# Kernel tuning notes

Hardware: AMD Instinct MI355X
Metric: run time of the kernel (lower is better)

## Reference

```python
import jax, jax.numpy as jnp
import numpy as np

WS = (7, 7)   # window size
SS = (3, 3)   # shift size
NH = 8        # num heads
DIM = 256
B_, H_, W_ = 16, 112, 112


def _rel_index(wh, ww):
    ch, cw = np.meshgrid(np.arange(wh), np.arange(ww), indexing='ij')
    cf = np.stack([ch, cw]).reshape(2, -1)
    rc = (cf[:, :, None] - cf[:, None, :]).transpose(1, 2, 0)
    rc[:, :, 0] += wh - 1
    rc[:, :, 1] += ww - 1
    rc[:, :, 0] *= 2 * ww - 1
    return rc.sum(-1).reshape(-1)


def _shift_mask(pH, pW, wh, ww, sh, sw):
    m = np.zeros((pH, pW))
    cnt = 0
    for h0, h1 in ((0, pH - wh), (pH - wh, pH - sh), (pH - sh, pH)):
        for w0, w1 in ((0, pW - ww), (pW - ww, pW - sw), (pW - sw, pW)):
            m[h0:h1, w0:w1] = cnt
            cnt += 1
    m = m.reshape(pH // wh, wh, pW // ww, ww).transpose(0, 2, 1, 3).reshape(-1, wh * ww)
    d = m[:, None, :] - m[:, :, None]  # (nW, N, N), [w,i,j] = m[w,j]-m[w,i]
    return np.where(d != 0, -100.0, 0.0).astype(np.float32)


def _partition(x, wh, ww):
    B, H, W, C = x.shape
    x = x.reshape(B, H // wh, wh, W // ww, ww, C).transpose(0, 1, 3, 2, 4, 5)
    return x.reshape(B * (H // wh) * (W // ww), wh * ww, C)


def _unpartition(x, B, H, W, wh, ww):
    C = x.shape[-1]
    x = x.reshape(B, H // wh, W // ww, wh, ww, C).transpose(0, 1, 3, 2, 4, 5)
    return x.reshape(B, H, W, C)


def setup_inputs() -> dict:
    key = jax.random.key(0)
    ks = jax.random.split(key, 12)
    D = DIM
    inp = {
        'Q': jax.random.normal(ks[0], (B_, H_, W_, D), jnp.float32),
        'K': jax.random.normal(ks[1], (B_, H_, W_, D), jnp.float32),
        'V': jax.random.normal(ks[2], (B_, H_, W_, D), jnp.float32),
        'Qw': jax.random.normal(ks[3], (D, D), jnp.float32) * 0.02,
        'Qb': jax.random.normal(ks[4], (D,), jnp.float32) * 0.02,
        'Kw': jax.random.normal(ks[5], (D, D), jnp.float32) * 0.02,
        'Kb': jax.random.normal(ks[6], (D,), jnp.float32) * 0.02,
        'Vw': jax.random.normal(ks[7], (D, D), jnp.float32) * 0.02,
        'Vb': jax.random.normal(ks[8], (D,), jnp.float32) * 0.02,
        'Pw': jax.random.normal(ks[9], (D, D), jnp.float32) * 0.02,
        'Pb': jax.random.normal(ks[10], (D,), jnp.float32) * 0.02,
        'rpb_table': jax.random.normal(ks[11], ((2 * WS[0] - 1) * (2 * WS[1] - 1), NH), jnp.float32) * 0.02,
        'rp_index': jnp.asarray(_rel_index(WS[0], WS[1]), jnp.int32),
    }
    return inp


def reference(Q, K, V, Qw, Qb, Kw, Kb, Vw, Vb, Pw, Pb, rpb_table, rp_index):
    wh, ww = WS
    nh = NH
    B, H, W, C = Q.shape
    N = wh * ww
    hd = C // nh
    pad_b = (wh - H % wh) % wh
    pad_r = (ww - W % ww) % ww
    if pad_b or pad_r:
        pad = ((0, 0), (0, pad_b), (0, pad_r), (0, 0))
        Q, K, V = jnp.pad(Q, pad), jnp.pad(K, pad), jnp.pad(V, pad)
    pH, pW = H + pad_b, W + pad_r
    sh = 0 if wh >= pH else SS[0]
    sw = 0 if ww >= pW else SS[1]
    shifted = (sh + sw) > 0
    if shifted:
        Q = jnp.roll(Q, (-sh, -sw), (1, 2))
        K = jnp.roll(K, (-sh, -sw), (1, 2))
        V = jnp.roll(V, (-sh, -sw), (1, 2))
    xq = _partition(Q, wh, ww)  # (B*nW, N, C)
    xk = _partition(K, wh, ww)
    xv = _partition(V, wh, ww)
    q = (xq @ Qw.T + Qb).reshape(-1, N, nh, hd).transpose(0, 2, 1, 3) * (hd ** -0.5)
    k = (xk @ Kw.T + Kb).reshape(-1, N, nh, hd).transpose(0, 2, 1, 3)
    v = (xv @ Vw.T + Vb).reshape(-1, N, nh, hd).transpose(0, 2, 1, 3)
    bias = rpb_table[rp_index].reshape(N, N, nh).transpose(2, 0, 1)  # (nh, N, N)
    attn = jnp.einsum('bhnd,bhmd->bhnm', q, k) + bias[None]
    if shifted:
        mask = jnp.asarray(_shift_mask(pH, pW, wh, ww, sh, sw))  # (nW, N, N)
        nW = (pH // wh) * (pW // ww)
        attn = attn.reshape(B, nW, nh, N, N) + mask[None, :, None]
        attn = attn.reshape(-1, nh, N, N)
    attn = jax.nn.softmax(attn, axis=-1)
    x = jnp.einsum('bhnm,bhmd->bhnd', attn, v).transpose(0, 2, 1, 3).reshape(-1, N, C)
    x = x @ Pw.T + Pb
    x = _unpartition(x, B, pH, pW, wh, ww)
    if shifted:
        x = jnp.roll(x, (sh, sw), (1, 2))
    return x[:, :H, :W, :]
```

## Files before the change

### kernel.cpp

```cpp
#include <hip/hip_runtime.h>


typedef short  bf16x4_t __attribute__((ext_vector_type(4)));
typedef short  bf16x8_t __attribute__((ext_vector_type(8)));
typedef float  f32x4_t  __attribute__((ext_vector_type(4)));
typedef int    i32x4_t  __attribute__((ext_vector_type(4)));

#define HH    112
#define WWDIM 112
#define NTOK  49
#define NWIN  4096
#define SHIFT 3

__device__ __forceinline__ unsigned short f2bf(float f) {
  unsigned u = __builtin_bit_cast(unsigned, f);
  u += 0x7FFFu + ((u >> 16) & 1u);
  return (unsigned short)(u >> 16);
}

__device__ __forceinline__ bf16x8_t ld8(const unsigned short* p) {
  return __builtin_bit_cast(bf16x8_t, *reinterpret_cast<const i32x4_t*>(p));
}

__device__ __forceinline__ bf16x4_t pack4(float a, float b, float c, float d) {
  union { unsigned short u[4]; bf16x4_t v; } t;
  t.u[0] = f2bf(a); t.u[1] = f2bf(b); t.u[2] = f2bf(c); t.u[3] = f2bf(d);
  return t.v;
}

__device__ __forceinline__ int swzi(int row, int col, int rowElems) {
  int by = col << 1;
  int sb = (((by >> 4) ^ (row & 7)) << 4) | (by & 15);
  return row * rowElems + (sb >> 1);
}

__global__ void prep_kernel(const float* __restrict__ Qw, const float* __restrict__ Kw,
                            const float* __restrict__ Vw, const float* __restrict__ Pw,
                            const float* __restrict__ rpb, const int* __restrict__ rpi,
                            unsigned short* __restrict__ wbf, float* __restrict__ biasT) {
  int idx = blockIdx.x * 256 + threadIdx.x;
  if (idx < 4 * 65536) {
    int which = idx >> 16, e = idx & 65535;
    const float* s = (which == 0) ? Qw : (which == 1) ? Kw : (which == 2) ? Vw : Pw;
    wbf[idx] = f2bf(s[e]);
  }
  if (idx < 8 * NTOK * NTOK) {
    int h = idx / (NTOK * NTOK), ij = idx % (NTOK * NTOK);
    int i = ij / NTOK, j = ij - (ij / NTOK) * NTOK;
    biasT[h * (NTOK * NTOK) + j * NTOK + i] = rpb[rpi[ij] * 8 + h];
  }
}

#define GLOAD(SRC)                                                            \
  do {                                                                        \
    _Pragma("unroll") for (int it = 0; it < 8; ++it) {                        \
      g[it] = ((wid + (it << 3)) < NTOK)                                      \
                  ? *reinterpret_cast<const float4*>((SRC) + goff[it])        \
                  : make_float4(0.f, 0.f, 0.f, 0.f);                          \
    }                                                                         \
  } while (0)

#define XWRITE()                                                              \
  do {                                                                        \
    _Pragma("unroll") for (int it = 0; it < 8; ++it) {                        \
      unsigned v0 = (unsigned)f2bf(g[it].x) | ((unsigned)f2bf(g[it].y) << 16);\
      unsigned v1 = (unsigned)f2bf(g[it].z) | ((unsigned)f2bf(g[it].w) << 16);\
      *reinterpret_cast<uint2*>(                                              \
          &Xs[swzi(wid + (it << 3), lane << 2, 256)]) = make_uint2(v0, v1);   \
    }                                                                         \
  } while (0)

#define WHOIST(PH)                                                            \
  do {                                                                        \
    const unsigned short* W_ = wbf + ((PH) << 16);                            \
    _Pragma("unroll") for (int ks = 0; ks < 8; ++ks)                          \
        _Pragma("unroll") for (int t = 0; t < 2; ++t)                         \
            bw[ks][t] =                                                       \
        ld8(&W_[(((wid << 5) + (t << 4) + lo) << 8) + (ks << 5) + kof]);      \
  } while (0)

__global__ __launch_bounds__(512, 2) void fused_kernel(
    const float* __restrict__ Qin, const float* __restrict__ Kin, const float* __restrict__ Vin,
    const float* __restrict__ Qbv, const float* __restrict__ Kbv, const float* __restrict__ Vbv,
    const float* __restrict__ Pbv,
    const unsigned short* __restrict__ wbf, const float* __restrict__ biasT,
    float* __restrict__ out) {
  __shared__ unsigned short Xs[64 * 256];

  const int blk = blockIdx.x, tid = threadIdx.x;
  const int lane = tid & 63, wid = tid >> 6;
  const int b = blk >> 8, wi = (blk >> 4) & 15, wj = blk & 15;
  const int lo = lane & 15, hi = lane >> 4;
  const int g4 = hi << 2, kof = hi << 3;

  unsigned goff[8];
#pragma unroll
  for (int it = 0; it < 8; ++it) {
    int row = wid + (it << 3);
    unsigned off = 0;
    if (row < NTOK) {
      int i = row / 7, j = row - i * 7;
      int h_ = wi * 7 + i + SHIFT; if (h_ >= HH) h_ -= HH;
      int w_ = wj * 7 + j + SHIFT; if (w_ >= WWDIM) w_ -= WWDIM;
      off = ((unsigned)((b * HH + h_) * WWDIM + w_) << 8) + (lane << 2);
    }
    goff[it] = off;
  }

  float4 g[8];
  bf16x8_t bw[8][2];
  bf16x4_t qf[2][4], kf[2][4], vf[4][2];

  GLOAD(Qin);
  WHOIST(0);
  XWRITE();
  __syncthreads();

#pragma unroll
  for (int ph = 0; ph < 2; ++ph) {
    GLOAD(ph == 0 ? Kin : Vin);
    f32x4_t acc[2][4];
#pragma unroll
    for (int a = 0; a < 2; ++a)
#pragma unroll
      for (int c = 0; c < 4; ++c) acc[a][c] = (f32x4_t){0.f, 0.f, 0.f, 0.f};
#pragma unroll
    for (int ks = 0; ks < 8; ++ks) {
      const int kk = (ks << 5) + kof;
      bf16x8_t xb[4];
#pragma unroll
      for (int nj = 0; nj < 4; ++nj) xb[nj] = ld8(&Xs[swzi((nj << 4) + lo, kk, 256)]);
#pragma unroll
      for (int mi = 0; mi < 2; ++mi)
#pragma unroll
        for (int nj = 0; nj < 4; ++nj)
          acc[mi][nj] = __builtin_amdgcn_mfma_f32_16x16x32_bf16(bw[ks][mi], xb[nj], acc[mi][nj], 0, 0, 0);
    }
    const float* bias = (ph == 0) ? Qbv : Kbv;
    const float scale = (ph == 0) ? 0.17677669529663687f : 1.0f;
    bf16x4_t (*dst)[4] = (ph == 0) ? qf : kf;
#pragma unroll
    for (int mi = 0; mi < 2; ++mi) {
      const float4 bb = *reinterpret_cast<const float4*>(bias + (wid << 5) + (mi << 4) + g4);
#pragma unroll
      for (int nj = 0; nj < 4; ++nj)
        dst[mi][nj] = pack4((acc[mi][nj][0] + bb.x) * scale, (acc[mi][nj][1] + bb.y) * scale,
                            (acc[mi][nj][2] + bb.z) * scale, (acc[mi][nj][3] + bb.w) * scale);
    }
    __syncthreads();
    WHOIST(ph + 1);
    XWRITE();
    __syncthreads();
  }

  {
    f32x4_t acc[4][2];
#pragma unroll
    for (int a = 0; a < 4; ++a)
#pragma unroll
      for (int c = 0; c < 2; ++c) acc[a][c] = (f32x4_t){0.f, 0.f, 0.f, 0.f};
#pragma unroll
    for (int ks = 0; ks < 8; ++ks) {
      const int kk = (ks << 5) + kof;
      bf16x8_t xa[4];
#pragma unroll
      for (int mi = 0; mi < 4; ++mi) xa[mi] = ld8(&Xs[swzi((mi << 4) + lo, kk, 256)]);
#pragma unroll
      for (int mi = 0; mi < 4; ++mi)
#pragma unroll
        for (int t = 0; t < 2; ++t)
          acc[mi][t] = __builtin_amdgcn_mfma_f32_16x16x32_bf16(xa[mi], bw[ks][t], acc[mi][t], 0, 0, 0);
    }
    float bbv[2];
#pragma unroll
    for (int t = 0; t < 2; ++t) bbv[t] = Vbv[(wid << 5) + (t << 4) + lo];
#pragma unroll
    for (int mi = 0; mi < 4; ++mi)
#pragma unroll
      for (int t = 0; t < 2; ++t)
        vf[mi][t] = pack4(acc[mi][t][0] + bbv[t], acc[mi][t][1] + bbv[t],
                          acc[mi][t][2] + bbv[t], acc[mi][t][3] + bbv[t]);
  }
  WHOIST(3);

  const bool wi15 = (wi == 15), wj15 = (wj == 15);
  unsigned kbi = 0, kbj = 0, kval = 0;
#pragma unroll
  for (int njk = 0; njk < 4; ++njk)
#pragma unroll
    for (int rg = 0; rg < 4; ++rg) {
      int kt = (njk << 4) + g4 + rg;
      if (kt < NTOK) {
        int ti = kt / 7, tj = kt - (kt / 7) * 7;
        unsigned bit = 1u << (njk * 4 + rg);
        kval |= bit;
        if (ti >= 4) kbi |= bit;
        if (tj >= 4) kbj |= bit;
      }
    }

  f32x4_t st[4][4];
  __builtin_amdgcn_s_setprio(1);
#pragma unroll
  for (int njk = 0; njk < 4; ++njk)
#pragma unroll
    for (int njq = 0; njq < 4; ++njq) {
      st[njk][njq] = __builtin_amdgcn_mfma_f32_16x16x16bf16_1k(
          kf[0][njk], qf[0][njq], (f32x4_t){0.f, 0.f, 0.f, 0.f}, 0, 0, 0);
      st[njk][njq] = __builtin_amdgcn_mfma_f32_16x16x16bf16_1k(
          kf[1][njk], qf[1][njq], st[njk][njq], 0, 0, 0);
    }
  __builtin_amdgcn_s_setprio(0);

  const float* bh = biasT + wid * (NTOK * NTOK);
  bf16x4_t pf[4][4];
#pragma unroll
  for (int njq = 0; njq < 4; ++njq) {
    const int qt = (njq << 4) + lo;
    const bool qv = qt < NTOK;
    const int sqt = qv ? qt : 0;
    const int qti = sqt / 7, qtj = sqt - (sqt / 7) * 7;
    const bool qbi = qti >= 4, qbj = qtj >= 4;
    float vals[4][4];
    float m = -3e38f;
#pragma unroll
    for (int njk = 0; njk < 4; ++njk)
#pragma unroll
      for (int rg = 0; rg < 4; ++rg) {
        const int bit = njk * 4 + rg;
        const int kt = (njk << 4) + g4 + rg;
        const bool valid = qv && ((kval >> bit) & 1u);
        float v = st[njk][njq][rg] + bh[(valid ? kt : 0) * NTOK + sqt];
        if (wi15 && (qbi != (bool)((kbi >> bit) & 1u))) v -= 100.f;
        if (wj15 && (qbj != (bool)((kbj >> bit) & 1u))) v -= 100.f;
        v = valid ? v : -1e30f;
        vals[njk][rg] = v;
        m = fmaxf(m, v);
      }
    m = fmaxf(m, __shfl_xor(m, 16));
    m = fmaxf(m, __shfl_xor(m, 32));
    float sum = 0.f;
#pragma unroll
    for (int njk = 0; njk < 4; ++njk)
#pragma unroll
      for (int rg = 0; rg < 4; ++rg) {
        const float e = __expf(vals[njk][rg] - m);
        vals[njk][rg] = e;
        sum += e;
      }
    sum += __shfl_xor(sum, 16);
    sum += __shfl_xor(sum, 32);
    const float inv = 1.f / sum;
#pragma unroll
    for (int njk = 0; njk < 4; ++njk)
      pf[njk][njq] = pack4(vals[njk][0] * inv, vals[njk][1] * inv,
                           vals[njk][2] * inv, vals[njk][3] * inv);
  }

  f32x4_t o[2][4];
#pragma unroll
  for (int a = 0; a < 2; ++a)
#pragma unroll
    for (int c = 0; c < 4; ++c) o[a][c] = (f32x4_t){0.f, 0.f, 0.f, 0.f};
  __builtin_amdgcn_s_setprio(1);
#pragma unroll
  for (int mi = 0; mi < 4; ++mi)
#pragma unroll
    for (int t = 0; t < 2; ++t)
#pragma unroll
      for (int njq = 0; njq < 4; ++njq)
        o[t][njq] = __builtin_amdgcn_mfma_f32_16x16x16bf16_1k(vf[mi][t], pf[mi][njq], o[t][njq], 0, 0, 0);
  __builtin_amdgcn_s_setprio(0);

  __syncthreads();
#pragma unroll
  for (int t = 0; t < 2; ++t)
#pragma unroll
    for (int njq = 0; njq < 4; ++njq) {
      const int qt = (njq << 4) + lo;
      const int ch0 = (wid << 5) + (t << 4) + g4;
      unsigned u0 = (unsigned)f2bf(o[t][njq][0]) | ((unsigned)f2bf(o[t][njq][1]) << 16);
      unsigned u1 = (unsigned)f2bf(o[t][njq][2]) | ((unsigned)f2bf(o[t][njq][3]) << 16);
      *reinterpret_cast<uint2*>(&Xs[swzi(qt, ch0, 256)]) = make_uint2(u0, u1);
    }
  __syncthreads();

  f32x4_t y[2][4];
#pragma unroll
  for (int a = 0; a < 2; ++a)
#pragma unroll
    for (int c = 0; c < 4; ++c) y[a][c] = (f32x4_t){0.f, 0.f, 0.f, 0.f};
#pragma unroll
  for (int ks = 0; ks < 8; ++ks) {
    const int kk = (ks << 5) + kof;
    bf16x8_t xb[4];
#pragma unroll
    for (int nj = 0; nj < 4; ++nj) xb[nj] = ld8(&Xs[swzi((nj << 4) + lo, kk, 256)]);
#pragma unroll
    for (int mi = 0; mi < 2; ++mi)
#pragma unroll
      for (int nj = 0; nj < 4; ++nj)
        y[mi][nj] = __builtin_amdgcn_mfma_f32_16x16x32_bf16(bw[ks][mi], xb[nj], y[mi][nj], 0, 0, 0);
  }
  float4 pb[2];
#pragma unroll
  for (int mi = 0; mi < 2; ++mi)
    pb[mi] = *reinterpret_cast<const float4*>(Pbv + (wid << 5) + (mi << 4) + g4);
#pragma unroll
  for (int nj = 0; nj < 4; ++nj) {
    const int tok = (nj << 4) + lo;
    if (tok < NTOK) {
      const int i = tok / 7, j = tok - (tok / 7) * 7;
      int h_ = wi * 7 + i + SHIFT; if (h_ >= HH) h_ -= HH;
      int w_ = wj * 7 + j + SHIFT; if (w_ >= WWDIM) w_ -= WWDIM;
      float* ob = out + ((size_t)((b * HH + h_) * WWDIM + w_) << 8);
#pragma unroll
      for (int mi = 0; mi < 2; ++mi) {
        const int ch0 = (wid << 5) + (mi << 4) + g4;
        *reinterpret_cast<float4*>(ob + ch0) =
            make_float4(y[mi][nj][0] + pb[mi].x, y[mi][nj][1] + pb[mi].y,
                        y[mi][nj][2] + pb[mi].z, y[mi][nj][3] + pb[mi].w);
      }
    }
  }
}

extern "C" void kernel_launch(void* const* d_in, const int* in_sizes, int n_in,
                              void* d_out, int out_size, void* d_ws, size_t ws_size,
                              hipStream_t stream) {
  const float* Q   = (const float*)d_in[0];
  const float* K   = (const float*)d_in[1];
  const float* V   = (const float*)d_in[2];
  const float* Qw  = (const float*)d_in[3];
  const float* Qb  = (const float*)d_in[4];
  const float* Kw  = (const float*)d_in[5];
  const float* Kb  = (const float*)d_in[6];
  const float* Vw  = (const float*)d_in[7];
  const float* Vb  = (const float*)d_in[8];
  const float* Pw  = (const float*)d_in[9];
  const float* Pb  = (const float*)d_in[10];
  const float* rpb = (const float*)d_in[11];
  const int*   rpi = (const int*)d_in[12];

  unsigned short* wbf = (unsigned short*)d_ws;
  float* biasT = (float*)(wbf + 4 * 65536);

  const size_t need = (size_t)4 * 65536 * 2 + (size_t)8 * NTOK * NTOK * 4;
  if (ws_size < need) return;

  prep_kernel<<<1024, 256, 0, stream>>>(Qw, Kw, Vw, Pw, rpb, rpi, wbf, biasT);
  fused_kernel<<<NWIN, 512, 0, stream>>>(Q, K, V, Qb, Kb, Vb, Pb, wbf, biasT,
                                         (float*)d_out);
}
```

Baseline: 459.6 us.

## Double-buffer LDS, use hardware bf16 pack/exp2, vectorize bias loads in softmax

Doubles the shared-memory staging buffer so the next input tile is written while the current one is read, removing one barrier per phase and the barrier before the output write. It replaces the software bf16 rounding with v_cvt_pk_bf16_f32 and the expf with v_exp_f32 by folding log2e into the q scale, bias and mask. It also uses a fast reciprocal and re-lays the relative-position bias as a padded, q-major table so each score tile loads it with float4 reads, computing scores per query tile. The doubled LDS (64KB per block) may reduce how many blocks fit per CU, and the changed rounding and exp path alter numerics slightly.

Measured after the change: 448.2 us. 1.03x faster.

```diff
diff --git a/kernel.cpp b/kernel.cpp
--- a/kernel.cpp
+++ b/kernel.cpp
@@ -11,6 +11,8 @@
 #define NTOK  49
 #define NWIN  4096
 #define SHIFT 3
+#define LOG2E 1.4426950408889634f
+#define MASKS (-144.26950408889634f)
 
 __device__ __forceinline__ unsigned short f2bf(float f) {
   unsigned u = __builtin_bit_cast(unsigned, f);
@@ -18,13 +20,25 @@
   return (unsigned short)(u >> 16);
 }
 
+__device__ __forceinline__ unsigned cvtpk(float a, float b) {
+  unsigned r;
+  asm("v_cvt_pk_bf16_f32 %0, %1, %2" : "=v"(r) : "v"(a), "v"(b));
+  return r;
+}
+
+__device__ __forceinline__ float exp2fast(float x) {
+  float r;
+  asm("v_exp_f32 %0, %1" : "=v"(r) : "v"(x));
+  return r;
+}
+
 __device__ __forceinline__ bf16x8_t ld8(const unsigned short* p) {
   return __builtin_bit_cast(bf16x8_t, *reinterpret_cast<const i32x4_t*>(p));
 }
 
 __device__ __forceinline__ bf16x4_t pack4(float a, float b, float c, float d) {
-  union { unsigned short u[4]; bf16x4_t v; } t;
-  t.u[0] = f2bf(a); t.u[1] = f2bf(b); t.u[2] = f2bf(c); t.u[3] = f2bf(d);
+  union { unsigned u[2]; bf16x4_t v; } t;
+  t.u[0] = cvtpk(a, b); t.u[1] = cvtpk(c, d);
   return t.v;
 }
 
@@ -37,17 +51,17 @@
 __global__ void prep_kernel(const float* __restrict__ Qw, const float* __restrict__ Kw,
                             const float* __restrict__ Vw, const float* __restrict__ Pw,
                             const float* __restrict__ rpb, const int* __restrict__ rpi,
-                            unsigned short* __restrict__ wbf, float* __restrict__ biasT) {
+                            unsigned short* __restrict__ wbf, float* __restrict__ biasP) {
   int idx = blockIdx.x * 256 + threadIdx.x;
   if (idx < 4 * 65536) {
     int which = idx >> 16, e = idx & 65535;
     const float* s = (which == 0) ? Qw : (which == 1) ? Kw : (which == 2) ? Vw : Pw;
     wbf[idx] = f2bf(s[e]);
   }
-  if (idx < 8 * NTOK * NTOK) {
-    int h = idx / (NTOK * NTOK), ij = idx % (NTOK * NTOK);
-    int i = ij / NTOK, j = ij - (ij / NTOK) * NTOK;
-    biasT[h * (NTOK * NTOK) + j * NTOK + i] = rpb[rpi[ij] * 8 + h];
+  if (idx < 8 * 49 * 64) {
+    int h = idx / 3136, r = idx - h * 3136;
+    int i = r >> 6, j = r & 63;
+    biasP[idx] = (i < NTOK && j < NTOK) ? rpb[rpi[i * NTOK + j] * 8 + h] * LOG2E : 0.f;
   }
 }
 
@@ -60,13 +74,13 @@
     }                                                                         \
   } while (0)
 
-#define XWRITE()                                                              \
+#define XWRITE(B)                                                             \
   do {                                                                        \
     _Pragma("unroll") for (int it = 0; it < 8; ++it) {                        \
-      unsigned v0 = (unsigned)f2bf(g[it].x) | ((unsigned)f2bf(g[it].y) << 16);\
-      unsigned v1 = (unsigned)f2bf(g[it].z) | ((unsigned)f2bf(g[it].w) << 16);\
+      unsigned v0 = cvtpk(g[it].x, g[it].y);                                  \
+      unsigned v1 = cvtpk(g[it].z, g[it].w);                                  \
       *reinterpret_cast<uint2*>(                                              \
-          &Xs[swzi(wid + (it << 3), lane << 2, 256)]) = make_uint2(v0, v1);   \
+          &Xs[B][swzi(wid + (it << 3), lane << 2, 256)]) = make_uint2(v0, v1);\
     }                                                                         \
   } while (0)
 
@@ -83,9 +97,9 @@
     const float* __restrict__ Qin, const float* __restrict__ Kin, const float* __restrict__ Vin,
     const float* __restrict__ Qbv, const float* __restrict__ Kbv, const float* __restrict__ Vbv,
     const float* __restrict__ Pbv,
-    const unsigned short* __restrict__ wbf, const float* __restrict__ biasT,
+    const unsigned short* __restrict__ wbf, const float* __restrict__ biasP,
     float* __restrict__ out) {
-  __shared__ unsigned short Xs[64 * 256];
+  __shared__ unsigned short Xs[2][64 * 256];
 
   const int blk = blockIdx.x, tid = threadIdx.x;
   const int lane = tid & 63, wid = tid >> 6;
@@ -112,13 +126,14 @@
   bf16x4_t qf[2][4], kf[2][4], vf[4][2];
 
   GLOAD(Qin);
+  XWRITE(0);
   WHOIST(0);
-  XWRITE();
   __syncthreads();
 
 #pragma unroll
   for (int ph = 0; ph < 2; ++ph) {
     GLOAD(ph == 0 ? Kin : Vin);
+    const unsigned short* Xb = Xs[ph];
     f32x4_t acc[2][4];
 #pragma unroll
     for (int a = 0; a < 2; ++a)
@@ -129,7 +144,7 @@
       const int kk = (ks << 5) + kof;
       bf16x8_t xb[4];
 #pragma unroll
-      for (int nj = 0; nj < 4; ++nj) xb[nj] = ld8(&Xs[swzi((nj << 4) + lo, kk, 256)]);
+      for (int nj = 0; nj < 4; ++nj) xb[nj] = ld8(&Xb[swzi((nj << 4) + lo, kk, 256)]);
 #pragma unroll
       for (int mi = 0; mi < 2; ++mi)
 #pragma unroll
@@ -137,7 +152,7 @@
           acc[mi][nj] = __builtin_amdgcn_mfma_f32_16x16x32_bf16(bw[ks][mi], xb[nj], acc[mi][nj], 0, 0, 0);
     }
     const float* bias = (ph == 0) ? Qbv : Kbv;
-    const float scale = (ph == 0) ? 0.17677669529663687f : 1.0f;
+    const float scale = (ph == 0) ? 0.17677669529663687f * LOG2E : 1.0f;
     bf16x4_t (*dst)[4] = (ph == 0) ? qf : kf;
 #pragma unroll
     for (int mi = 0; mi < 2; ++mi) {
@@ -147,13 +162,13 @@
         dst[mi][nj] = pack4((acc[mi][nj][0] + bb.x) * scale, (acc[mi][nj][1] + bb.y) * scale,
                             (acc[mi][nj][2] + bb.z) * scale, (acc[mi][nj][3] + bb.w) * scale);
     }
+    XWRITE(ph ^ 1);
+    WHOIST(ph + 1);
     __syncthreads();
-    WHOIST(ph + 1);
-    XWRITE();
-    __syncthreads();
   }
 
   {
+    const unsigned short* Xb = Xs[0];
     f32x4_t acc[4][2];
 #pragma unroll
     for (int a = 0; a < 4; ++a)
@@ -164,7 +179,7 @@
       const int kk = (ks << 5) + kof;
       bf16x8_t xa[4];
 #pragma unroll
-      for (int mi = 0; mi < 4; ++mi) xa[mi] = ld8(&Xs[swzi((mi << 4) + lo, kk, 256)]);
+      for (int mi = 0; mi < 4; ++mi) xa[mi] = ld8(&Xb[swzi((mi << 4) + lo, kk, 256)]);
 #pragma unroll
       for (int mi = 0; mi < 4; ++mi)
 #pragma unroll
@@ -199,26 +214,29 @@
       }
     }
 
-  f32x4_t st[4][4];
-  __builtin_amdgcn_s_setprio(1);
-#pragma unroll
-  for (int njk = 0; njk < 4; ++njk)
-#pragma unroll
-    for (int njq = 0; njq < 4; ++njq) {
-      st[njk][njq] = __builtin_amdgcn_mfma_f32_16x16x16bf16_1k(
-          kf[0][njk], qf[0][njq], (f32x4_t){0.f, 0.f, 0.f, 0.f}, 0, 0, 0);
-      st[njk][njq] = __builtin_amdgcn_mfma_f32_16x16x16bf16_1k(
-          kf[1][njk], qf[1][njq], st[njk][njq], 0, 0, 0);
-    }
-  __builtin_amdgcn_s_setprio(0);
-
-  const float* bh = biasT + wid * (NTOK * NTOK);
   bf16x4_t pf[4][4];
 #pragma unroll
   for (int njq = 0; njq < 4; ++njq) {
     const int qt = (njq << 4) + lo;
     const bool qv = qt < NTOK;
     const int sqt = qv ? qt : 0;
+    const float* bq = biasP + wid * 3136 + (sqt << 6);
+    f32x4_t bfr[4];
+#pragma unroll
+    for (int njk = 0; njk < 4; ++njk)
+      bfr[njk] = *reinterpret_cast<const f32x4_t*>(bq + (njk << 4) + g4);
+
+    f32x4_t stc[4];
+    __builtin_amdgcn_s_setprio(1);
+#pragma unroll
+    for (int njk = 0; njk < 4; ++njk) {
+      stc[njk] = __builtin_amdgcn_mfma_f32_16x16x16bf16_1k(
+          kf[0][njk], qf[0][njq], (f32x4_t){0.f, 0.f, 0.f, 0.f}, 0, 0, 0);
+      stc[njk] = __builtin_amdgcn_mfma_f32_16x16x16bf16_1k(
+          kf[1][njk], qf[1][njq], stc[njk], 0, 0, 0);
+    }
+    __builtin_amdgcn_s_setprio(0);
+
     const int qti = sqt / 7, qtj = sqt - (sqt / 7) * 7;
     const bool qbi = qti >= 4, qbj = qtj >= 4;
     float vals[4][4];
@@ -228,11 +246,10 @@
 #pragma unroll
       for (int rg = 0; rg < 4; ++rg) {
         const int bit = njk * 4 + rg;
-        const int kt = (njk << 4) + g4 + rg;
         const bool valid = qv && ((kval >> bit) & 1u);
-        float v = st[njk][njq][rg] + bh[(valid ? kt : 0) * NTOK + sqt];
-        if (wi15 && (qbi != (bool)((kbi >> bit) & 1u))) v -= 100.f;
-        if (wj15 && (qbj != (bool)((kbj >> bit) & 1u))) v -= 100.f;
+        float v = stc[njk][rg] + bfr[njk][rg];
+        if (wi15 && (qbi != (bool)((kbi >> bit) & 1u))) v += MASKS;
+        if (wj15 && (qbj != (bool)((kbj >> bit) & 1u))) v += MASKS;
         v = valid ? v : -1e30f;
         vals[njk][rg] = v;
         m = fmaxf(m, v);
@@ -244,13 +261,13 @@
     for (int njk = 0; njk < 4; ++njk)
 #pragma unroll
       for (int rg = 0; rg < 4; ++rg) {
-        const float e = __expf(vals[njk][rg] - m);
+        const float e = exp2fast(vals[njk][rg] - m);
         vals[njk][rg] = e;
         sum += e;
       }
     sum += __shfl_xor(sum, 16);
     sum += __shfl_xor(sum, 32);
-    const float inv = 1.f / sum;
+    const float inv = __builtin_amdgcn_rcpf(sum);
 #pragma unroll
     for (int njk = 0; njk < 4; ++njk)
       pf[njk][njq] = pack4(vals[njk][0] * inv, vals[njk][1] * inv,
@@ -272,54 +289,55 @@
         o[t][njq] = __builtin_amdgcn_mfma_f32_16x16x16bf16_1k(vf[mi][t], pf[mi][njq], o[t][njq], 0, 0, 0);
   __builtin_amdgcn_s_setprio(0);
 
-  __syncthreads();
 #pragma unroll
   for (int t = 0; t < 2; ++t)
 #pragma unroll
     for (int njq = 0; njq < 4; ++njq) {
       const int qt = (njq << 4) + lo;
       const int ch0 = (wid << 5) + (t << 4) + g4;
-      unsigned u0 = (unsigned)f2bf(o[t][njq][0]) | ((unsigned)f2bf(o[t][njq][1]) << 16);
-      unsigned u1 = (unsigned)f2bf(o[t][njq][2]) | ((unsigned)f2bf(o[t][njq][3]) << 16);
-      *reinterpret_cast<uint2*>(&Xs[swzi(qt, ch0, 256)]) = make_uint2(u0, u1);
+      *reinterpret_cast<uint2*>(&Xs[1][swzi(qt, ch0, 256)]) =
+          make_uint2(cvtpk(o[t][njq][0], o[t][njq][1]), cvtpk(o[t][njq][2], o[t][njq][3]));
     }
   __syncthreads();
 
-  f32x4_t y[2][4];
-#pragma unroll
-  for (int a = 0; a < 2; ++a)
-#pragma unroll
-    for (int c = 0; c < 4; ++c) y[a][c] = (f32x4_t){0.f, 0.f, 0.f, 0.f};
-#pragma unroll
-  for (int ks = 0; ks < 8; ++ks) {
-    const int kk = (ks << 5) + kof;
-    bf16x8_t xb[4];
-#pragma unroll
-    for (int nj = 0; nj < 4; ++nj) xb[nj] = ld8(&Xs[swzi((nj << 4) + lo, kk, 256)]);
+  {
+    const unsigned short* Xb = Xs[1];
+    f32x4_t y[2][4];
+#pragma unroll
+    for (int a = 0; a < 2; ++a)
+#pragma unroll
+      for (int c = 0; c < 4; ++c) y[a][c] = (f32x4_t){0.f, 0.f, 0.f, 0.f};
+#pragma unroll
+    for (int ks = 0; ks < 8; ++ks) {
+      const int kk = (ks << 5) + kof;
+      bf16x8_t xb[4];
+#pragma unroll
+      for (int nj = 0; nj < 4; ++nj) xb[nj] = ld8(&Xb[swzi((nj << 4) + lo, kk, 256)]);
+#pragma unroll
+      for (int mi = 0; mi < 2; ++mi)
+#pragma unroll
+        for (int nj = 0; nj < 4; ++nj)
+          y[mi][nj] = __builtin_amdgcn_mfma_f32_16x16x32_bf16(bw[ks][mi], xb[nj], y[mi][nj], 0, 0, 0);
+    }
+    float4 pb[2];
 #pragma unroll
     for (int mi = 0; mi < 2; ++mi)
-#pragma unroll
-      for (int nj = 0; nj < 4; ++nj)
-        y[mi][nj] = __builtin_amdgcn_mfma_f32_16x16x32_bf16(bw[ks][mi], xb[nj], y[mi][nj], 0, 0, 0);
-  }
-  float4 pb[2];
-#pragma unroll
-  for (int mi = 0; mi < 2; ++mi)
-    pb[mi] = *reinterpret_cast<const float4*>(Pbv + (wid << 5) + (mi << 4) + g4);
-#pragma unroll
-  for (int nj = 0; nj < 4; ++nj) {
-    const int tok = (nj << 4) + lo;
-    if (tok < NTOK) {
-      const int i = tok / 7, j = tok - (tok / 7) * 7;
-      int h_ = wi * 7 + i + SHIFT; if (h_ >= HH) h_ -= HH;
-      int w_ = wj * 7 + j + SHIFT; if (w_ >= WWDIM) w_ -= WWDIM;
-      float* ob = out + ((size_t)((b * HH + h_) * WWDIM + w_) << 8);
-#pragma unroll
-      for (int mi = 0; mi < 2; ++mi) {
-        const int ch0 = (wid << 5) + (mi << 4) + g4;
-        *reinterpret_cast<float4*>(ob + ch0) =
-            make_float4(y[mi][nj][0] + pb[mi].x, y[mi][nj][1] + pb[mi].y,
-                        y[mi][nj][2] + pb[mi].z, y[mi][nj][3] + pb[mi].w);
+      pb[mi] = *reinterpret_cast<const float4*>(Pbv + (wid << 5) + (mi << 4) + g4);
+#pragma unroll
+    for (int nj = 0; nj < 4; ++nj) {
+      const int tok = (nj << 4) + lo;
+      if (tok < NTOK) {
+        const int i = tok / 7, j = tok - (tok / 7) * 7;
+        int h_ = wi * 7 + i + SHIFT; if (h_ >= HH) h_ -= HH;
+        int w_ = wj * 7 + j + SHIFT; if (w_ >= WWDIM) w_ -= WWDIM;
+        float* ob = out + ((size_t)((b * HH + h_) * WWDIM + w_) << 8);
+#pragma unroll
+        for (int mi = 0; mi < 2; ++mi) {
+          const int ch0 = (wid << 5) + (mi << 4) + g4;
+          *reinterpret_cast<float4*>(ob + ch0) =
+              make_float4(y[mi][nj][0] + pb[mi].x, y[mi][nj][1] + pb[mi].y,
+                          y[mi][nj][2] + pb[mi].z, y[mi][nj][3] + pb[mi].w);
+        }
       }
     }
   }
@@ -343,12 +361,12 @@
   const int*   rpi = (const int*)d_in[12];
 
   unsigned short* wbf = (unsigned short*)d_ws;
-  float* biasT = (float*)(wbf + 4 * 65536);
-
-  const size_t need = (size_t)4 * 65536 * 2 + (size_t)8 * NTOK * NTOK * 4;
+  float* biasP = (float*)(wbf + 4 * 65536);
+
+  const size_t need = (size_t)4 * 65536 * 2 + (size_t)8 * 49 * 64 * 4;
   if (ws_size < need) return;
 
-  prep_kernel<<<1024, 256, 0, stream>>>(Qw, Kw, Vw, Pw, rpb, rpi, wbf, biasT);
-  fused_kernel<<<NWIN, 512, 0, stream>>>(Q, K, V, Qb, Kb, Vb, Pb, wbf, biasT,
+  prep_kernel<<<1024, 256, 0, stream>>>(Qw, Kw, Vw, Pw, rpb, rpi, wbf, biasP);
+  fused_kernel<<<NWIN, 512, 0, stream>>>(Q, K, V, Qb, Kb, Vb, Pb, wbf, biasP,
                                          (float*)d_out);
 }
```
